# Kernel optimization log

Hardware: AMD Instinct MI355X
Metric: run time of the kernel (lower is better)

The kernel has to match this reference:

```python
import jax, jax.numpy as jnp
import numpy as np
from jax.scipy.special import gammaln

T_STEPS, N_GRID, NMUL = 730, 10000, 2
NEARZERO = 1e-5
LENF = 15  # unit-hydrograph length used by UH_gamma routing
STAT_NAMES = ["parFC", "parK0", "parK1", "parK2", "parLP", "parPERC", "parUZL",
              "parTT", "parCFMAX", "parCFR", "parCWH", "parC", "parRT", "parAC"]
BOUNDS = {"parBETA": (1.0, 6.0), "parFC": (50.0, 1000.0), "parK0": (0.05, 0.9),
          "parK1": (0.01, 0.5), "parK2": (0.001, 0.2), "parLP": (0.2, 1.0),
          "parPERC": (0.0, 10.0), "parUZL": (0.0, 100.0), "parTT": (-2.5, 2.5),
          "parCFMAX": (0.5, 10.0), "parCFR": (0.0, 0.1), "parCWH": (0.0, 0.2),
          "parBETAET": (0.3, 5.0), "parC": (0.0, 1.0), "parRT": (0.0, 20.0),
          "parAC": (0.0, 2500.0)}
ROUT_A = (0.0, 2.9)
ROUT_B = (0.0, 6.5)


def _scale(p, lo, hi):
    # change_param_range: affine map of [0,1]-normalized params to physical bounds
    return p * (hi - lo) + lo


def setup_inputs() -> dict:
    key = jax.random.key(0)
    ks = jax.random.split(key, 7)
    prcp = jax.random.uniform(ks[0], (T_STEPS, N_GRID)) * 10.0          # mm/day
    tmean = jax.random.uniform(ks[1], (T_STEPS, N_GRID)) * 30.0 - 10.0  # deg C, spans parTT range
    pet = jax.random.uniform(ks[2], (T_STEPS, N_GRID)) * 5.0            # mm/day
    x_phy = jnp.stack([prcp, tmean, pet], axis=-1).astype(jnp.float32)
    ac_all = jax.random.uniform(ks[3], (N_GRID,)) * 2500.0              # drainage area per unit basin
    elev_all = jax.random.uniform(ks[4], (N_GRID,)) * 3000.0            # elevation
    params_dy = jax.random.uniform(ks[5], (T_STEPS, N_GRID, 2 * NMUL))  # dynamic: parBETA, parBETAET
    params_stat = jax.random.uniform(ks[6], (N_GRID, 14 * NMUL + 2))    # 14 static phy + 2 routing
    return {"x_phy": x_phy, "ac_all": ac_all, "elev_all": elev_all,
            "params_dy": params_dy, "params_stat": params_stat}


def _forward(x_phy, ac_all, elev_all, params_dy, params_stat):
    T, G, _ = x_phy.shape
    P, Tair, PET = x_phy[..., 0], x_phy[..., 1], x_phy[..., 2]
    # expand forcing to nmul parameter components
    Pm = jnp.broadcast_to(P[..., None], (T, G, NMUL))
    Tm = jnp.broadcast_to(Tair[..., None], (T, G, NMUL))
    PETm = jnp.broadcast_to(PET[..., None], (T, G, NMUL))
    Ac = jnp.broadcast_to(ac_all[:, None], (G, NMUL))

    # dynamic (per-timestep) params; dy_drop=0.0 -> bernoulli drop mask is all zeros,
    # so the dynamic values are used directly at every step
    dy = params_dy.reshape(T, G, 2, NMUL)
    parBETA = _scale(dy[:, :, 0], *BOUNDS["parBETA"])
    parBETAET = _scale(dy[:, :, 1], *BOUNDS["parBETAET"])

    # static params: [G, 14, NMUL]
    stat = params_stat[:, :14 * NMUL].reshape(G, 14, NMUL)
    sp = {n: _scale(stat[:, i], *BOUNDS[n]) for i, n in enumerate(STAT_NAMES)}
    rout_a = _scale(params_stat[:, 14 * NMUL], *ROUT_A)
    rout_b = _scale(params_stat[:, 14 * NMUL + 1], *ROUT_B)

    def step(carry, xt):
        SNOWPACK, MELTWATER, SM, SUZ, SLZ = carry
        Pt, Tt, PETt, beta, betaet = xt
        rain_mask = (Tt >= sp["parTT"]).astype(Pt.dtype)
        RAIN = Pt * rain_mask
        SNOW = Pt * (1.0 - rain_mask)
        # --- snow bucket ---
        SNOWPACK = SNOWPACK + SNOW
        melt = jnp.maximum(sp["parCFMAX"] * (Tt - sp["parTT"]), 0.0)
        melt = jnp.minimum(melt, SNOWPACK)
        MELTWATER = MELTWATER + melt
        SNOWPACK = SNOWPACK - melt
        refreeze = jnp.maximum(sp["parCFR"] * sp["parCFMAX"] * (sp["parTT"] - Tt), 0.0)
        refreeze = jnp.minimum(refreeze, MELTWATER)
        SNOWPACK = SNOWPACK + refreeze
        MELTWATER = MELTWATER - refreeze
        tosoil = jnp.maximum(MELTWATER - sp["parCWH"] * SNOWPACK, 0.0)
        MELTWATER = MELTWATER - tosoil
        # --- soil bucket ---
        soil_wetness = jnp.clip((SM / sp["parFC"]) ** beta, 0.0, 1.0)
        recharge = (RAIN + tosoil) * soil_wetness
        SM = SM + RAIN + tosoil - recharge
        excess = jnp.maximum(SM - sp["parFC"], 0.0)
        SM = SM - excess
        evapfactor = jnp.clip(SM / (sp["parLP"] * sp["parFC"]), 0.0, 1.0) ** betaet
        ETact = jnp.minimum(SM, PETt * evapfactor)
        SM = jnp.maximum(SM - ETact, NEARZERO)
        # capillary rise from lower groundwater zone (parC)
        capillary = jnp.minimum(SLZ, sp["parC"] * SLZ * (1.0 - jnp.minimum(SM / sp["parFC"], 1.0)))
        SM = jnp.maximum(SM + capillary, NEARZERO)
        SLZ = jnp.maximum(SLZ - capillary, NEARZERO)
        # --- groundwater buckets ---
        SUZ = SUZ + recharge + excess
        PERC = jnp.minimum(SUZ, sp["parPERC"])
        SUZ = SUZ - PERC
        Q0 = sp["parK0"] * jnp.maximum(SUZ - sp["parUZL"], 0.0)
        SUZ = SUZ - Q0
        Q1 = sp["parK1"] * SUZ
        SUZ = SUZ - Q1
        SLZ = SLZ + PERC
        # HBV 2.0 regional groundwater loss (area-dependent via parRT / parAC; reconstructed)
        gw_loss = jnp.minimum(SLZ, sp["parRT"] * jnp.clip(1.0 - Ac / (sp["parAC"] + NEARZERO), 0.0, 1.0))
        SLZ = SLZ - gw_loss
        Q2 = sp["parK2"] * SLZ
        SLZ = SLZ - Q2
        Qt = Q0 + Q1 + Q2
        return (SNOWPACK, MELTWATER, SM, SUZ, SLZ), Qt

    init = tuple(jnp.full((G, NMUL), 1e-3, dtype=x_phy.dtype) for _ in range(5))
    _, Qsimmu = jax.lax.scan(step, init, (Pm, Tm, PETm, parBETA, parBETAET))
    Qsim = Qsimmu.mean(-1)  # [T, G]; muwts=None -> uniform average over nmul components

    # --- gamma unit-hydrograph routing (UH_gamma + causal UH_conv) ---
    a = jnp.maximum(rout_a, 0.0) + 0.1       # [G]
    theta = jnp.maximum(rout_b, 0.0) + 0.5   # [G]
    t = jnp.arange(LENF, dtype=Qsim.dtype) + 0.5  # [LENF]
    w = (jnp.exp(-gammaln(a))[None, :] * theta[None, :] ** (-a[None, :])
         * t[:, None] ** (a[None, :] - 1.0) * jnp.exp(-t[:, None] / theta[None, :]))
    w = w / w.sum(0)  # [LENF, G], normalized UH weights
    # causal grouped conv: flow[t] = sum_k w[k] * Qsim[t-k]
    Qpad = jnp.pad(Qsim, ((LENF - 1, 0), (0, 0)))
    flow = jnp.zeros_like(Qsim)
    for k in range(LENF):  # fixed, small tap count
        flow = flow + w[k][None, :] * Qpad[LENF - 1 - k: LENF - 1 - k + T]
    return flow[..., None]  # [T, G, 1] routed streamflow


def reference(x_phy, ac_all, elev_all, params_dy, params_stat):
    return _forward(x_phy, ac_all, elev_all, params_dy, params_stat)
```

## Files before the change

kernel.cpp:

```cpp
#include <hip/hip_runtime.h>


#define TS 730
#define NG 10000
#define CH 15
#define NCHUNK 49
#define XSTRIDE (NG * 3)
#define DSTRIDE (NG * 4)

#define AS1 __attribute__((address_space(1)))
#define AS3 __attribute__((address_space(3)))
#define WAIT_VMCNT(n) __builtin_amdgcn_s_waitcnt(((n) & 15) | 0x70 | 0xF00 | (((n) >> 4) << 14))
#define WAIT_LGKM0    __builtin_amdgcn_s_waitcnt(0xC07F)
#define SBAR          __builtin_amdgcn_s_barrier
#define SCHED_FENCE() __builtin_amdgcn_sched_barrier(0)

__device__ __forceinline__ void gload16(const float* g, float* l) {
    __builtin_amdgcn_global_load_lds((const AS1 void*)g, (AS3 void*)l, 16, 0, 0);
}
__device__ __forceinline__ float powpos(float x, float b) {
    return __builtin_amdgcn_exp2f(b * __builtin_amdgcn_logf(x));
}
__device__ __forceinline__ float med3(float x, float lo, float hi) {
    return __builtin_amdgcn_fmed3f(x, lo, hi);
}

__global__ __launch_bounds__(192, 1) void hbv_fused(
    const float* __restrict__ x_phy,
    const float* __restrict__ ac_all,
    const float* __restrict__ params_dy,
    const float* __restrict__ params_stat,
    float* __restrict__ out)
{
    __shared__ float xls0[1536], xls1[1536], xls2[1536], xls3[1536];
    __shared__ float dls0[2048], dls1[2048], dls2[2048], dls3[2048];
    __shared__ float rb0[960], rb1[960];
    __shared__ float qb0[960], qb1[960];

    const int tid  = threadIdx.x;
    const int wid  = tid >> 6;
    const int lane = tid & 63;
    const int m    = lane >> 5;
    const int cell = lane & 31;
    const int g0   = blockIdx.x * 32;
    const int g    = g0 + cell;
    const int gl   = g < NG ? g : NG - 1;
    const int g0r  = (g0 <= NG - 32) ? g0 : NG - 32;
    const int co   = cell + (g0 - g0r);
    const int cl   = co < 31 ? co : 31;

    const float* ps = params_stat + (size_t)gl * 30;
    const float FC    = ps[0  + m] * 950.f   + 50.f;
    const float K0    = ps[2  + m] * 0.85f   + 0.05f;
    const float K1    = ps[4  + m] * 0.49f   + 0.01f;
    const float K2    = ps[6  + m] * 0.199f  + 0.001f;
    const float LP    = ps[8  + m] * 0.8f    + 0.2f;
    const float PERCp = ps[10 + m] * 10.f;
    const float UZL   = ps[12 + m] * 100.f;
    const float TTp   = ps[14 + m] * 5.f     - 2.5f;
    const float CFMAX = ps[16 + m] * 9.5f    + 0.5f;
    const float CFR   = ps[18 + m] * 0.1f;
    const float CWH   = ps[20 + m] * 0.2f;
    const float Cc    = ps[22 + m];
    const float RT    = ps[24 + m] * 20.f;
    const float ACp   = ps[26 + m] * 2500.f;

    const float Acv     = ac_all[gl];
    const float invFC   = 1.f / FC;
    const float invLPFC = 1.f / (LP * FC);
    const float nCFRC   = -(CFR * CFMAX);
    const float gwcap   = RT * fminf(fmaxf(1.f - Acv / (ACp + 1e-5f), 0.f), 1.f);

    if (wid == 0) {
        float SP = 1e-3f, MW = 1e-3f;
        auto snowc = [&](const float* xl, float* rbuf) {
            float Pc = xl[cl * 3 + 0], Tc = xl[cl * 3 + 1];
#pragma unroll
            for (int j = 0; j < CH; ++j) {
                float Pn, Tn;
                if (j < CH - 1) {
                    Pn = xl[(j + 1) * 96 + cl * 3 + 0];
                    Tn = xl[(j + 1) * 96 + cl * 3 + 1];
                }
                const float t1   = Tc - TTp;
                const float snow = (t1 < 0.f) ? Pc : 0.f;
                const float rain = Pc - snow;
                SP += snow;
                const float melt = med3(CFMAX * t1, 0.f, SP);
                MW += melt; SP -= melt;
                const float refr = med3(nCFRC * t1, 0.f, MW);
                SP += refr; MW -= refr;
                const float tosoil = fmaxf(MW - CWH * SP, 0.f);
                MW -= tosoil;
                rbuf[(j << 6) + lane] = rain + tosoil;
                Pc = Pn; Tc = Tn;
            }
        };
        SBAR();
        for (int cq = 0; cq < 12; ++cq) {
            snowc(xls0, rb0); WAIT_LGKM0; SCHED_FENCE(); SBAR();
            snowc(xls1, rb1); WAIT_LGKM0; SCHED_FENCE(); SBAR();
            snowc(xls2, rb0); WAIT_LGKM0; SCHED_FENCE(); SBAR();
            snowc(xls3, rb1); WAIT_LGKM0; SCHED_FENCE(); SBAR();
        }
        snowc(xls0, rb0); WAIT_LGKM0; SCHED_FENCE(); SBAR();
        SBAR();
    } else if (wid == 1) {
        float SM = 1e-3f, SUZ = 1e-3f, SLZ = 1e-3f;
        float CcSLZ = Cc * 1e-3f;
        auto soilc = [&](const float* xl, const float* dl,
                         const float* rbuf, float* qbuf) {
            float Ec   = xl[cl * 3 + 2];
            float4 dvc = *(const float4*)&dl[cl * 4];
            float rtsc = rbuf[lane];
#pragma unroll
            for (int j = 0; j < CH; ++j) {
                float En, rtsn; float4 dvn;
                if (j < CH - 1) {
                    En   = xl[(j + 1) * 96 + cl * 3 + 2];
                    dvn  = *(const float4*)&dl[(j + 1) * 128 + cl * 4];
                    rtsn = rbuf[((j + 1) << 6) + lane];
                }
                const float beta   = fmaf(m ? dvc.y : dvc.x, 5.f, 1.f);
                const float betaet = fmaf(m ? dvc.w : dvc.z, 4.7f, 0.3f);

                const float sw  = fminf(powpos(SM * invFC, beta), 1.f);
                const float rts = rtsc;
                SM = fmaf(rts, 1.f - sw, SM);
                const float exc = fmaxf(SM - FC, 0.f);
                SM = fminf(SM, FC);
                const float ef = powpos(fminf(SM * invLPFC, 1.f), betaet);
                SM = fmaxf(SM - Ec * ef, 1e-5f);
                const float cap = CcSLZ * fmaxf(1.f - SM * invFC, 0.f);
                SM  = fmaxf(SM + cap, 1e-5f);
                SLZ = fmaxf(SLZ - cap, 1e-5f);

                SUZ = SUZ + rts * sw + exc;
                const float perc = fminf(SUZ, PERCp);
                SUZ -= perc;
                const float Q0 = K0 * fmaxf(SUZ - UZL, 0.f);
                SUZ -= Q0;
                const float Q1 = K1 * SUZ;
                SUZ -= Q1;
                SLZ += perc;
                SLZ = fmaxf(SLZ - gwcap, 0.f);
                const float Q2 = K2 * SLZ;
                SLZ -= Q2;
                CcSLZ = Cc * SLZ;
                qbuf[(j << 6) + lane] = Q0 + Q1 + Q2;

                Ec = En; dvc = dvn; rtsc = rtsn;
            }
        };
        SBAR();
        SBAR();
        for (int cq = 0; cq < 12; ++cq) {
            soilc(xls0, dls0, rb0, qb0); WAIT_LGKM0; SCHED_FENCE(); SBAR();
            soilc(xls1, dls1, rb1, qb1); WAIT_LGKM0; SCHED_FENCE(); SBAR();
            soilc(xls2, dls2, rb0, qb0); WAIT_LGKM0; SCHED_FENCE(); SBAR();
            soilc(xls3, dls3, rb1, qb1); WAIT_LGKM0; SCHED_FENCE(); SBAR();
        }
        soilc(xls0, dls0, rb0, qb0); WAIT_LGKM0; SCHED_FENCE(); SBAR();
    } else {
        const float ra = ps[28] * 2.9f;
        const float rb = ps[29] * 6.5f;
        const float a    = fmaxf(ra, 0.f) + 0.1f;
        const float th   = fmaxf(rb, 0.f) + 0.5f;
        const float am1  = a - 1.f;
        const float nl2e = 1.44269504f / th;
        float w[CH];
        float wsum = 0.f;
#pragma unroll
        for (int k = 0; k < CH; ++k) {
            const float tk = (float)k + 0.5f;
            const float v  = __builtin_amdgcn_exp2f(am1 * __builtin_amdgcn_logf(tk) - tk * nl2e);
            w[k] = v; wsum += v;
        }
        const float wn = 0.5f / wsum;
#pragma unroll
        for (int k = 0; k < CH; ++k) w[k] *= wn;

        int offx[6], offd[8];
#pragma unroll
        for (int i = 0; i < 6; ++i) {
            int idx = i * 64 + lane;
            idx = idx < 360 ? idx : 359;
            const int row = idx / 24;
            const int col = idx - row * 24;
            offx[i] = row * XSTRIDE + col * 4;
        }
#pragma unroll
        for (int i = 0; i < 8; ++i) {
            int idx = i * 64 + lane;
            idx = idx < 480 ? idx : 479;
            const int row = idx >> 5;
            const int col = idx & 31;
            offd[i] = row * DSTRIDE + col * 4;
        }
        const float* xbase = x_phy     + (size_t)g0r * 3;
        const float* dbase = params_dy + (size_t)g0r * 4;

        auto issue = [&](int cc, float* xl, float* dl) {
            if (cc == NCHUNK - 1) {
#pragma unroll
                for (int i = 0; i < 6; ++i) {
                    int idx = i * 64 + lane; idx = idx < 360 ? idx : 359;
                    const int row = idx / 24, col = idx - row * 24;
                    int t = cc * CH + row; t = t < TS ? t : TS - 1;
                    gload16(xbase + (size_t)t * XSTRIDE + col * 4, xl + i * 256);
                }
#pragma unroll
                for (int i = 0; i < 8; ++i) {
                    int idx = i * 64 + lane; idx = idx < 480 ? idx : 479;
                    const int row = idx >> 5, col = idx & 31;
                    int t = cc * CH + row; t = t < TS ? t : TS - 1;
                    gload16(dbase + (size_t)t * DSTRIDE + col * 4, dl + i * 256);
                }
            } else {
                const float* xp = xbase + (size_t)cc * CH * XSTRIDE;
                const float* dp = dbase + (size_t)cc * CH * DSTRIDE;
#pragma unroll
                for (int i = 0; i < 6; ++i) gload16(xp + offx[i], xl + i * 256);
#pragma unroll
                for (int i = 0; i < 8; ++i) gload16(dp + offd[i], dl + i * 256);
            }
        };

        float facc[CH];
#pragma unroll
        for (int k = 0; k < CH; ++k) facc[k] = 0.f;
        const bool doStore = (g < NG);
        const int  l32 = cell;

        auto conv = [&](int c, const float* qb) {
            float* op = out + (size_t)c * CH * NG + g;
            const int tb = c * CH;
#pragma unroll
            for (int j = 0; j < CH; ++j) {
                const float qm = qb[(j << 6) + l32] + qb[(j << 6) + 32 + l32];
#pragma unroll
                for (int k = 0; k < CH; ++k)
                    facc[(j + k) % CH] = fmaf(w[k], qm, facc[(j + k) % CH]);
                if (doStore && (lane < 32) && (tb + j < TS))
                    op[(size_t)j * NG] = facc[j];
                facc[j] = 0.f;
            }
        };

        issue(0, xls0, dls0);
        issue(1, xls1, dls1);
        WAIT_VMCNT(14); SCHED_FENCE(); SBAR();
        issue(2, xls2, dls2);
        WAIT_VMCNT(14); SCHED_FENCE(); SBAR();
        issue(3, xls3, dls3);
        WAIT_VMCNT(14); SCHED_FENCE(); SBAR();
        issue(4, xls0, dls0); conv(0, qb0);
        WAIT_VMCNT(29); SCHED_FENCE(); SBAR();
        for (int np = 0; np < 11; ++np) {
            const int n = 3 + 4 * np;
            issue(n + 2, xls1, dls1); conv(n - 2, qb1);
            WAIT_VMCNT(44); SCHED_FENCE(); SBAR();
            issue(n + 3, xls2, dls2); conv(n - 1, qb0);
            WAIT_VMCNT(44); SCHED_FENCE(); SBAR();
            issue(n + 4, xls3, dls3); conv(n,     qb1);
            WAIT_VMCNT(44); SCHED_FENCE(); SBAR();
            issue(n + 5, xls0, dls0); conv(n + 1, qb0);
            WAIT_VMCNT(44); SCHED_FENCE(); SBAR();
        }
        conv(45, qb1);
        WAIT_VMCNT(30); SCHED_FENCE(); SBAR();
        conv(46, qb0); SBAR();
        conv(47, qb1); SBAR();
        conv(48, qb0);
    }
}

extern "C" void kernel_launch(void* const* d_in, const int* in_sizes, int n_in,
                              void* d_out, int out_size, void* d_ws, size_t ws_size,
                              hipStream_t stream) {
    const float* x_phy = (const float*)d_in[0];
    const float* ac    = (const float*)d_in[1];
    const float* pdy   = (const float*)d_in[3];
    const float* pst   = (const float*)d_in[4];
    float* out = (float*)d_out;

    const int grid = (NG + 31) / 32;
    hbv_fused<<<grid, 192, 0, stream>>>(x_phy, ac, pdy, pst, out);
}
```

Measured before the change: 258.7 us.

## Process 64 cells per block with each lane handling both nmul components

Each block now covers 64 grid cells instead of 32. Each lane in the snow and soil waves runs both parameter components (nmul=2) as two independent recurrences, so the grid shrinks to about half as many blocks. The loader and convolution waves are resized to match: more global-to-LDS loads per chunk, larger shared buffers, and adjusted vmcnt waits. The intent is more instruction-level parallelism per lane and less per-block overhead, at the cost of twice the serial work per lane and fewer blocks than CUs, which can leave hardware idle.

```diff
diff --git a/kernel.cpp b/kernel.cpp
--- a/kernel.cpp
+++ b/kernel.cpp
@@ -7,6 +7,7 @@
 #define NCHUNK 49
 #define XSTRIDE (NG * 3)
 #define DSTRIDE (NG * 4)
+#define CELLS 64
 
 #define AS1 __attribute__((address_space(1)))
 #define AS3 __attribute__((address_space(3)))
@@ -32,140 +33,149 @@
     const float* __restrict__ params_stat,
     float* __restrict__ out)
 {
-    __shared__ float xls0[1536], xls1[1536], xls2[1536], xls3[1536];
-    __shared__ float dls0[2048], dls1[2048], dls2[2048], dls3[2048];
-    __shared__ float rb0[960], rb1[960];
-    __shared__ float qb0[960], qb1[960];
+    __shared__ float xls0[3072], xls1[3072], xls2[3072], xls3[3072];
+    __shared__ float dls0[3840], dls1[3840], dls2[3840], dls3[3840];
+    __shared__ float rbA[1920], rbB[1920];
+    __shared__ float qbA[1920], qbB[1920];
 
     const int tid  = threadIdx.x;
     const int wid  = tid >> 6;
     const int lane = tid & 63;
-    const int m    = lane >> 5;
-    const int cell = lane & 31;
-    const int g0   = blockIdx.x * 32;
-    const int g    = g0 + cell;
-    const int gl   = g < NG ? g : NG - 1;
-    const int g0r  = (g0 <= NG - 32) ? g0 : NG - 32;
-    const int co   = cell + (g0 - g0r);
-    const int cl   = co < 31 ? co : 31;
-
-    const float* ps = params_stat + (size_t)gl * 30;
-    const float FC    = ps[0  + m] * 950.f   + 50.f;
-    const float K0    = ps[2  + m] * 0.85f   + 0.05f;
-    const float K1    = ps[4  + m] * 0.49f   + 0.01f;
-    const float K2    = ps[6  + m] * 0.199f  + 0.001f;
-    const float LP    = ps[8  + m] * 0.8f    + 0.2f;
-    const float PERCp = ps[10 + m] * 10.f;
-    const float UZL   = ps[12 + m] * 100.f;
-    const float TTp   = ps[14 + m] * 5.f     - 2.5f;
-    const float CFMAX = ps[16 + m] * 9.5f    + 0.5f;
-    const float CFR   = ps[18 + m] * 0.1f;
-    const float CWH   = ps[20 + m] * 0.2f;
-    const float Cc    = ps[22 + m];
-    const float RT    = ps[24 + m] * 20.f;
-    const float ACp   = ps[26 + m] * 2500.f;
-
-    const float Acv     = ac_all[gl];
-    const float invFC   = 1.f / FC;
-    const float invLPFC = 1.f / (LP * FC);
-    const float nCFRC   = -(CFR * CFMAX);
-    const float gwcap   = RT * fminf(fmaxf(1.f - Acv / (ACp + 1e-5f), 0.f), 1.f);
+    const int g0   = blockIdx.x * CELLS;
+    const int g0r  = (g0 <= NG - CELLS) ? g0 : NG - CELLS;
+    const int gcell = g0r + lane;
+
+    const float* psl = params_stat + (size_t)gcell * 30;
 
     if (wid == 0) {
-        float SP = 1e-3f, MW = 1e-3f;
+        float TTp[2], CFMAXv[2], nCFRC[2], CWHv[2], SP[2], MW[2];
+#pragma unroll
+        for (int mm = 0; mm < 2; ++mm) {
+            TTp[mm]    = psl[14 + mm] * 5.f   - 2.5f;
+            CFMAXv[mm] = psl[16 + mm] * 9.5f  + 0.5f;
+            nCFRC[mm]  = -(psl[18 + mm] * 0.1f * CFMAXv[mm]);
+            CWHv[mm]   = psl[20 + mm] * 0.2f;
+            SP[mm] = 1e-3f; MW[mm] = 1e-3f;
+        }
         auto snowc = [&](const float* xl, float* rbuf) {
-            float Pc = xl[cl * 3 + 0], Tc = xl[cl * 3 + 1];
+            float Pc = xl[lane * 3 + 0], Tc = xl[lane * 3 + 1];
 #pragma unroll
             for (int j = 0; j < CH; ++j) {
                 float Pn, Tn;
                 if (j < CH - 1) {
-                    Pn = xl[(j + 1) * 96 + cl * 3 + 0];
-                    Tn = xl[(j + 1) * 96 + cl * 3 + 1];
-                }
-                const float t1   = Tc - TTp;
-                const float snow = (t1 < 0.f) ? Pc : 0.f;
-                const float rain = Pc - snow;
-                SP += snow;
-                const float melt = med3(CFMAX * t1, 0.f, SP);
-                MW += melt; SP -= melt;
-                const float refr = med3(nCFRC * t1, 0.f, MW);
-                SP += refr; MW -= refr;
-                const float tosoil = fmaxf(MW - CWH * SP, 0.f);
-                MW -= tosoil;
-                rbuf[(j << 6) + lane] = rain + tosoil;
+                    Pn = xl[(j + 1) * 192 + lane * 3 + 0];
+                    Tn = xl[(j + 1) * 192 + lane * 3 + 1];
+                }
+#pragma unroll
+                for (int mm = 0; mm < 2; ++mm) {
+                    const float t1   = Tc - TTp[mm];
+                    const float snow = (t1 < 0.f) ? Pc : 0.f;
+                    const float rain = Pc - snow;
+                    SP[mm] += snow;
+                    const float melt = med3(CFMAXv[mm] * t1, 0.f, SP[mm]);
+                    MW[mm] += melt; SP[mm] -= melt;
+                    const float refr = med3(nCFRC[mm] * t1, 0.f, MW[mm]);
+                    SP[mm] += refr; MW[mm] -= refr;
+                    const float tosoil = fmaxf(MW[mm] - CWHv[mm] * SP[mm], 0.f);
+                    MW[mm] -= tosoil;
+                    rbuf[(j << 7) + (mm << 6) + lane] = rain + tosoil;
+                }
                 Pc = Pn; Tc = Tn;
             }
         };
         SBAR();
         for (int cq = 0; cq < 12; ++cq) {
-            snowc(xls0, rb0); WAIT_LGKM0; SCHED_FENCE(); SBAR();
-            snowc(xls1, rb1); WAIT_LGKM0; SCHED_FENCE(); SBAR();
-            snowc(xls2, rb0); WAIT_LGKM0; SCHED_FENCE(); SBAR();
-            snowc(xls3, rb1); WAIT_LGKM0; SCHED_FENCE(); SBAR();
-        }
-        snowc(xls0, rb0); WAIT_LGKM0; SCHED_FENCE(); SBAR();
+            snowc(xls0, rbA); WAIT_LGKM0; SCHED_FENCE(); SBAR();
+            snowc(xls1, rbB); WAIT_LGKM0; SCHED_FENCE(); SBAR();
+            snowc(xls2, rbA); WAIT_LGKM0; SCHED_FENCE(); SBAR();
+            snowc(xls3, rbB); WAIT_LGKM0; SCHED_FENCE(); SBAR();
+        }
+        snowc(xls0, rbA); WAIT_LGKM0; SCHED_FENCE(); SBAR();
         SBAR();
     } else if (wid == 1) {
-        float SM = 1e-3f, SUZ = 1e-3f, SLZ = 1e-3f;
-        float CcSLZ = Cc * 1e-3f;
+        float FCv[2], invFC[2], invLPFC[2], K0v[2], K1v[2], K2v[2],
+              PERCv[2], UZLv[2], gwc[2], Ccv[2];
+        float SM[2], SUZ[2], SLZ[2], CcSLZ[2];
+        const float Acv = ac_all[gcell];
+#pragma unroll
+        for (int mm = 0; mm < 2; ++mm) {
+            FCv[mm]   = psl[0  + mm] * 950.f  + 50.f;
+            K0v[mm]   = psl[2  + mm] * 0.85f  + 0.05f;
+            K1v[mm]   = psl[4  + mm] * 0.49f  + 0.01f;
+            K2v[mm]   = psl[6  + mm] * 0.199f + 0.001f;
+            const float LP = psl[8 + mm] * 0.8f + 0.2f;
+            PERCv[mm] = psl[10 + mm] * 10.f;
+            UZLv[mm]  = psl[12 + mm] * 100.f;
+            Ccv[mm]   = psl[22 + mm];
+            const float RT  = psl[24 + mm] * 20.f;
+            const float ACp = psl[26 + mm] * 2500.f;
+            invFC[mm]   = 1.f / FCv[mm];
+            invLPFC[mm] = 1.f / (LP * FCv[mm]);
+            gwc[mm] = RT * fminf(fmaxf(1.f - Acv / (ACp + 1e-5f), 0.f), 1.f);
+            SM[mm] = 1e-3f; SUZ[mm] = 1e-3f; SLZ[mm] = 1e-3f;
+            CcSLZ[mm] = Ccv[mm] * 1e-3f;
+        }
         auto soilc = [&](const float* xl, const float* dl,
                          const float* rbuf, float* qbuf) {
-            float Ec   = xl[cl * 3 + 2];
-            float4 dvc = *(const float4*)&dl[cl * 4];
-            float rtsc = rbuf[lane];
+            float Ec    = xl[lane * 3 + 2];
+            float4 dvc  = *(const float4*)&dl[lane * 4];
+            float rts0c = rbuf[lane], rts1c = rbuf[64 + lane];
 #pragma unroll
             for (int j = 0; j < CH; ++j) {
-                float En, rtsn; float4 dvn;
+                float En, rts0n, rts1n; float4 dvn;
                 if (j < CH - 1) {
-                    En   = xl[(j + 1) * 96 + cl * 3 + 2];
-                    dvn  = *(const float4*)&dl[(j + 1) * 128 + cl * 4];
-                    rtsn = rbuf[((j + 1) << 6) + lane];
-                }
-                const float beta   = fmaf(m ? dvc.y : dvc.x, 5.f, 1.f);
-                const float betaet = fmaf(m ? dvc.w : dvc.z, 4.7f, 0.3f);
-
-                const float sw  = fminf(powpos(SM * invFC, beta), 1.f);
-                const float rts = rtsc;
-                SM = fmaf(rts, 1.f - sw, SM);
-                const float exc = fmaxf(SM - FC, 0.f);
-                SM = fminf(SM, FC);
-                const float ef = powpos(fminf(SM * invLPFC, 1.f), betaet);
-                SM = fmaxf(SM - Ec * ef, 1e-5f);
-                const float cap = CcSLZ * fmaxf(1.f - SM * invFC, 0.f);
-                SM  = fmaxf(SM + cap, 1e-5f);
-                SLZ = fmaxf(SLZ - cap, 1e-5f);
-
-                SUZ = SUZ + rts * sw + exc;
-                const float perc = fminf(SUZ, PERCp);
-                SUZ -= perc;
-                const float Q0 = K0 * fmaxf(SUZ - UZL, 0.f);
-                SUZ -= Q0;
-                const float Q1 = K1 * SUZ;
-                SUZ -= Q1;
-                SLZ += perc;
-                SLZ = fmaxf(SLZ - gwcap, 0.f);
-                const float Q2 = K2 * SLZ;
-                SLZ -= Q2;
-                CcSLZ = Cc * SLZ;
-                qbuf[(j << 6) + lane] = Q0 + Q1 + Q2;
-
-                Ec = En; dvc = dvn; rtsc = rtsn;
+                    En    = xl[(j + 1) * 192 + lane * 3 + 2];
+                    dvn   = *(const float4*)&dl[(j + 1) * 256 + lane * 4];
+                    rts0n = rbuf[((j + 1) << 7) + lane];
+                    rts1n = rbuf[((j + 1) << 7) + 64 + lane];
+                }
+#pragma unroll
+                for (int mm = 0; mm < 2; ++mm) {
+                    const float beta   = fmaf(mm ? dvc.y : dvc.x, 5.f, 1.f);
+                    const float betaet = fmaf(mm ? dvc.w : dvc.z, 4.7f, 0.3f);
+                    const float rts    = mm ? rts1c : rts0c;
+
+                    const float sw = fminf(powpos(SM[mm] * invFC[mm], beta), 1.f);
+                    SM[mm] = fmaf(rts, 1.f - sw, SM[mm]);
+                    const float exc = fmaxf(SM[mm] - FCv[mm], 0.f);
+                    SM[mm] = fminf(SM[mm], FCv[mm]);
+                    const float ef = powpos(fminf(SM[mm] * invLPFC[mm], 1.f), betaet);
+                    SM[mm] = fmaxf(SM[mm] - Ec * ef, 1e-5f);
+                    const float cap = CcSLZ[mm] * fmaxf(1.f - SM[mm] * invFC[mm], 0.f);
+                    SM[mm]  = fmaxf(SM[mm] + cap, 1e-5f);
+                    SLZ[mm] = fmaxf(SLZ[mm] - cap, 1e-5f);
+
+                    SUZ[mm] = SUZ[mm] + rts * sw + exc;
+                    const float perc = fminf(SUZ[mm], PERCv[mm]);
+                    SUZ[mm] -= perc;
+                    const float Q0 = K0v[mm] * fmaxf(SUZ[mm] - UZLv[mm], 0.f);
+                    SUZ[mm] -= Q0;
+                    const float Q1 = K1v[mm] * SUZ[mm];
+                    SUZ[mm] -= Q1;
+                    SLZ[mm] += perc;
+                    SLZ[mm] = fmaxf(SLZ[mm] - gwc[mm], 0.f);
+                    const float Q2 = K2v[mm] * SLZ[mm];
+                    SLZ[mm] -= Q2;
+                    CcSLZ[mm] = Ccv[mm] * SLZ[mm];
+                    qbuf[(j << 7) + (mm << 6) + lane] = Q0 + Q1 + Q2;
+                }
+                Ec = En; dvc = dvn; rts0c = rts0n; rts1c = rts1n;
             }
         };
         SBAR();
         SBAR();
         for (int cq = 0; cq < 12; ++cq) {
-            soilc(xls0, dls0, rb0, qb0); WAIT_LGKM0; SCHED_FENCE(); SBAR();
-            soilc(xls1, dls1, rb1, qb1); WAIT_LGKM0; SCHED_FENCE(); SBAR();
-            soilc(xls2, dls2, rb0, qb0); WAIT_LGKM0; SCHED_FENCE(); SBAR();
-            soilc(xls3, dls3, rb1, qb1); WAIT_LGKM0; SCHED_FENCE(); SBAR();
-        }
-        soilc(xls0, dls0, rb0, qb0); WAIT_LGKM0; SCHED_FENCE(); SBAR();
+            soilc(xls0, dls0, rbA, qbA); WAIT_LGKM0; SCHED_FENCE(); SBAR();
+            soilc(xls1, dls1, rbB, qbB); WAIT_LGKM0; SCHED_FENCE(); SBAR();
+            soilc(xls2, dls2, rbA, qbA); WAIT_LGKM0; SCHED_FENCE(); SBAR();
+            soilc(xls3, dls3, rbB, qbB); WAIT_LGKM0; SCHED_FENCE(); SBAR();
+        }
+        soilc(xls0, dls0, rbA, qbA); WAIT_LGKM0; SCHED_FENCE(); SBAR();
     } else {
-        const float ra = ps[28] * 2.9f;
-        const float rb = ps[29] * 6.5f;
+        const float ra  = psl[28] * 2.9f;
+        const float rbp = psl[29] * 6.5f;
         const float a    = fmaxf(ra, 0.f) + 0.1f;
-        const float th   = fmaxf(rb, 0.f) + 0.5f;
+        const float th   = fmaxf(rbp, 0.f) + 0.5f;
         const float am1  = a - 1.f;
         const float nl2e = 1.44269504f / th;
         float w[CH];
@@ -180,21 +190,17 @@
 #pragma unroll
         for (int k = 0; k < CH; ++k) w[k] *= wn;
 
-        int offx[6], offd[8];
-#pragma unroll
-        for (int i = 0; i < 6; ++i) {
-            int idx = i * 64 + lane;
-            idx = idx < 360 ? idx : 359;
-            const int row = idx / 24;
-            const int col = idx - row * 24;
+        int offx[12], offd[15];
+#pragma unroll
+        for (int i = 0; i < 12; ++i) {
+            int idx = i * 64 + lane; idx = idx < 720 ? idx : 719;
+            const int row = idx / 48, col = idx - row * 48;
             offx[i] = row * XSTRIDE + col * 4;
         }
 #pragma unroll
-        for (int i = 0; i < 8; ++i) {
-            int idx = i * 64 + lane;
-            idx = idx < 480 ? idx : 479;
-            const int row = idx >> 5;
-            const int col = idx & 31;
+        for (int i = 0; i < 15; ++i) {
+            const int idx = i * 64 + lane;
+            const int row = idx >> 6, col = idx & 63;
             offd[i] = row * DSTRIDE + col * 4;
         }
         const float* xbase = x_phy     + (size_t)g0r * 3;
@@ -203,16 +209,16 @@
         auto issue = [&](int cc, float* xl, float* dl) {
             if (cc == NCHUNK - 1) {
 #pragma unroll
-                for (int i = 0; i < 6; ++i) {
-                    int idx = i * 64 + lane; idx = idx < 360 ? idx : 359;
-                    const int row = idx / 24, col = idx - row * 24;
+                for (int i = 0; i < 12; ++i) {
+                    int idx = i * 64 + lane; idx = idx < 720 ? idx : 719;
+                    const int row = idx / 48, col = idx - row * 48;
                     int t = cc * CH + row; t = t < TS ? t : TS - 1;
                     gload16(xbase + (size_t)t * XSTRIDE + col * 4, xl + i * 256);
                 }
 #pragma unroll
-                for (int i = 0; i < 8; ++i) {
-                    int idx = i * 64 + lane; idx = idx < 480 ? idx : 479;
-                    const int row = idx >> 5, col = idx & 31;
+                for (int i = 0; i < 15; ++i) {
+                    const int idx = i * 64 + lane;
+                    const int row = idx >> 6, col = idx & 63;
                     int t = cc * CH + row; t = t < TS ? t : TS - 1;
                     gload16(dbase + (size_t)t * DSTRIDE + col * 4, dl + i * 256);
                 }
@@ -220,58 +226,55 @@
                 const float* xp = xbase + (size_t)cc * CH * XSTRIDE;
                 const float* dp = dbase + (size_t)cc * CH * DSTRIDE;
 #pragma unroll
-                for (int i = 0; i < 6; ++i) gload16(xp + offx[i], xl + i * 256);
-#pragma unroll
-                for (int i = 0; i < 8; ++i) gload16(dp + offd[i], dl + i * 256);
+                for (int i = 0; i < 12; ++i) gload16(xp + offx[i], xl + i * 256);
+#pragma unroll
+                for (int i = 0; i < 15; ++i) gload16(dp + offd[i], dl + i * 256);
             }
         };
 
         float facc[CH];
 #pragma unroll
         for (int k = 0; k < CH; ++k) facc[k] = 0.f;
-        const bool doStore = (g < NG);
-        const int  l32 = cell;
+        const bool doStore = (gcell >= g0);
 
         auto conv = [&](int c, const float* qb) {
-            float* op = out + (size_t)c * CH * NG + g;
+            float* op = out + (size_t)c * CH * NG + gcell;
             const int tb = c * CH;
 #pragma unroll
             for (int j = 0; j < CH; ++j) {
-                const float qm = qb[(j << 6) + l32] + qb[(j << 6) + 32 + l32];
+                const float qm = qb[(j << 7) + lane] + qb[(j << 7) + 64 + lane];
 #pragma unroll
                 for (int k = 0; k < CH; ++k)
                     facc[(j + k) % CH] = fmaf(w[k], qm, facc[(j + k) % CH]);
-                if (doStore && (lane < 32) && (tb + j < TS))
-                    op[(size_t)j * NG] = facc[j];
+                if (doStore && (tb + j < TS)) op[(size_t)j * NG] = facc[j];
                 facc[j] = 0.f;
             }
         };
 
-        issue(0, xls0, dls0);
-        issue(1, xls1, dls1);
-        WAIT_VMCNT(14); SCHED_FENCE(); SBAR();
+        issue(0, xls0, dls0); issue(1, xls1, dls1);
+        WAIT_VMCNT(27); SCHED_FENCE(); SBAR();
         issue(2, xls2, dls2);
-        WAIT_VMCNT(14); SCHED_FENCE(); SBAR();
+        WAIT_VMCNT(27); SCHED_FENCE(); SBAR();
         issue(3, xls3, dls3);
-        WAIT_VMCNT(14); SCHED_FENCE(); SBAR();
-        issue(4, xls0, dls0); conv(0, qb0);
-        WAIT_VMCNT(29); SCHED_FENCE(); SBAR();
+        WAIT_VMCNT(27); SCHED_FENCE(); SBAR();
+        issue(4, xls0, dls0); conv(0, qbA);
+        WAIT_VMCNT(42); SCHED_FENCE(); SBAR();
         for (int np = 0; np < 11; ++np) {
-            const int n = 3 + 4 * np;
-            issue(n + 2, xls1, dls1); conv(n - 2, qb1);
-            WAIT_VMCNT(44); SCHED_FENCE(); SBAR();
-            issue(n + 3, xls2, dls2); conv(n - 1, qb0);
-            WAIT_VMCNT(44); SCHED_FENCE(); SBAR();
-            issue(n + 4, xls3, dls3); conv(n,     qb1);
-            WAIT_VMCNT(44); SCHED_FENCE(); SBAR();
-            issue(n + 5, xls0, dls0); conv(n + 1, qb0);
-            WAIT_VMCNT(44); SCHED_FENCE(); SBAR();
-        }
-        conv(45, qb1);
+            const int n = 4 + 4 * np;
+            issue(n + 1, xls1, dls1); conv(n - 3, qbB);
+            WAIT_VMCNT(42); SCHED_FENCE(); SBAR();
+            issue(n + 2, xls2, dls2); conv(n - 2, qbA);
+            WAIT_VMCNT(42); SCHED_FENCE(); SBAR();
+            issue(n + 3, xls3, dls3); conv(n - 1, qbB);
+            WAIT_VMCNT(42); SCHED_FENCE(); SBAR();
+            issue(n + 4, xls0, dls0); conv(n,     qbA);
+            WAIT_VMCNT(42); SCHED_FENCE(); SBAR();
+        }
+        conv(45, qbB);
         WAIT_VMCNT(30); SCHED_FENCE(); SBAR();
-        conv(46, qb0); SBAR();
-        conv(47, qb1); SBAR();
-        conv(48, qb0);
+        conv(46, qbA); SBAR();
+        conv(47, qbB); SBAR();
+        conv(48, qbA);
     }
 }
 
@@ -284,6 +287,6 @@
     const float* pst   = (const float*)d_in[4];
     float* out = (float*)d_out;
 
-    const int grid = (NG + 31) / 32;
+    const int grid = (NG + CELLS - 1) / CELLS;
     hbv_fused<<<grid, 192, 0, stream>>>(x_phy, ac, pdy, pst, out);
 }
```

Result: slower. 353.8 us (+36.7%).
